# Kernel tuning notes

Measured on AMD Instinct MI355X. Metric: run time of the kernel, lower is better.

The kernel has to match this reference:

```python
import jax, jax.numpy as jnp
import numpy as np

NUM_HEADS = 8
MAX_REL = 32  # max_relative_positions
LN_EPS = 1e-5


def _conv1x1(x, W, b):
    # x: (B, C, H, W), W: (Cout, Cin), b: (Cout,)
    return jnp.einsum('bchw,oc->bohw', x, W) + b[None, :, None, None]


def setup_inputs() -> dict:
    key = jax.random.key(0)
    ks = jax.random.split(key, 10)
    B, C, H, W = 2, 512, 48, 48
    L = H * W
    s = 1.0 / np.sqrt(C)
    inp = {
        'x': jax.random.normal(ks[0], (B, C, H, W), jnp.float32),
        'mask': jax.random.randint(ks[1], (1, NUM_HEADS, L, L), 0, 2).astype(bool),
        'learnable_pos': jax.random.normal(ks[2], (1, C, H, W), jnp.float32) * 0.02,
        'Wq': jax.random.normal(ks[3], (C, C), jnp.float32) * s,
        'bq': jnp.zeros((C,), jnp.float32),
        'Wk': jax.random.normal(ks[4], (C, C), jnp.float32) * s,
        'bk': jnp.zeros((C,), jnp.float32),
        'Wv': jax.random.normal(ks[5], (C, C), jnp.float32) * s,
        'bv': jnp.zeros((C,), jnp.float32),
        'Wo': jax.random.normal(ks[6], (C, C), jnp.float32) * s,
        'bo': jnp.zeros((C,), jnp.float32),
        'rel_table': jax.random.normal(ks[7], (NUM_HEADS, 2 * MAX_REL + 1), jnp.float32) * 0.02,
        'ln_gamma': jnp.ones((C,), jnp.float32),
        'ln_beta': jnp.zeros((C,), jnp.float32),
    }
    return inp


def reference(x, mask, learnable_pos, Wq, bq, Wk, bk, Wv, bv, Wo, bo,
              rel_table, ln_gamma, ln_beta):
    B, C, H, W = x.shape
    L = H * W
    hd = C // NUM_HEADS
    residual = x

    xp = x + learnable_pos
    q = _conv1x1(xp, Wq, bq)
    k = _conv1x1(xp, Wk, bk)
    v = _conv1x1(xp, Wv, bv)

    def split_heads(t):  # (B,C,H,W) -> (B, heads, L, hd)
        return t.reshape(B, NUM_HEADS, hd, L).transpose(0, 1, 3, 2)

    q, k, v = split_heads(q), split_heads(k), split_heads(v)

    scale = 1.0 / np.sqrt(hd).astype(np.float32)
    scores = jnp.einsum('bhld,bhmd->bhlm', q, k) * scale  # (B,H,L,L)

    # relative positional bias per head
    pos = jnp.arange(L)
    rp = jnp.clip(pos[:, None] - pos[None, :], -MAX_REL, MAX_REL) + MAX_REL  # (L,L)
    scores = scores + rel_table[:, rp][None]  # (1,heads,L,L) broadcast

    scores = jnp.where(mask, scores, jnp.float32(-1e9))
    attn = jax.nn.softmax(scores, axis=-1)

    out = jnp.einsum('bhlm,bhmd->bhld', attn, v)  # (B,heads,L,hd)
    out = out.transpose(0, 1, 3, 2).reshape(B, C, H, W)
    out = _conv1x1(out, Wo, bo)

    y = residual + out
    # LayerNorm over channels (channels-last permute in original)
    yl = y.transpose(0, 2, 3, 1)  # (B,H,W,C)
    mu = jnp.mean(yl, axis=-1, keepdims=True)
    var = jnp.var(yl, axis=-1, keepdims=True)
    yl = (yl - mu) * jax.lax.rsqrt(var + LN_EPS) * ln_gamma + ln_beta
    return yl.transpose(0, 3, 1, 2)
```

## Files before the change

kernel.cpp:

```cpp
#include <hip/hip_runtime.h>
#include <cstdint>

#define L_SEQ 2304
#define CDIM  512
#define NHEADS 8
#define HD    64
#define LL    ((size_t)L_SEQ * L_SEQ)
#define ROWS_TOT (16 * L_SEQ)
#define PERBL ((size_t)2 * L_SEQ * 512)

typedef short  s8v  __attribute__((ext_vector_type(8)));
typedef float  f4v  __attribute__((ext_vector_type(4)));

__device__ __forceinline__ ushort f2bf(float f) {
    union { float f; uint32_t u; } v; v.f = f;
    uint32_t u = v.u;
    uint32_t r = (u + 0x7FFFu + ((u >> 16) & 1u)) >> 16;
    return (ushort)r;
}

__device__ __forceinline__ float bf2f(ushort u) {
    union { uint32_t u; float f; } v; v.u = (uint32_t)u << 16;
    return v.f;
}

__global__ __launch_bounds__(256) void prep_w(
    const float* __restrict__ Wq, const float* __restrict__ Wk,
    const float* __restrict__ Wv, const float* __restrict__ Wo,
    ushort* __restrict__ wb)
{
    const int i   = blockIdx.x * 256 + threadIdx.x;
    const int mat = i >> 16;
    const int j   = i & 65535;
    const float* src = (mat == 0) ? Wq : (mat == 1) ? Wk : (mat == 2) ? Wv : Wo;
    const float4 w = ((const float4*)src)[j];
    ushort4 o;
    o.x = f2bf(w.x); o.y = f2bf(w.y); o.z = f2bf(w.z); o.w = f2bf(w.w);
    ((ushort4*)(wb + (size_t)mat * 262144))[j] = o;
}

__global__ __launch_bounds__(256) void xpose(
    const float* __restrict__ x, const float* __restrict__ pos,
    ushort* __restrict__ xt)
{
    __shared__ ushort T[64][72];
    const int l0 = blockIdx.x * 64;
    const int c0 = blockIdx.y * 64;
    const int b  = blockIdx.z;
    const int t  = threadIdx.x;
    const int cc = t >> 2;
    const int l4 = (t & 3) * 16;
    const size_t off  = ((size_t)b * CDIM + c0 + cc) * L_SEQ + l0 + l4;
    const size_t poff = (size_t)(c0 + cc) * L_SEQ + l0 + l4;
    #pragma unroll
    for (int j4 = 0; j4 < 4; j4++) {
        const float4 xv = *(const float4*)&x[off + j4 * 4];
        const float4 pv = *(const float4*)&pos[poff + j4 * 4];
        T[cc][l4 + j4 * 4 + 0] = f2bf(xv.x + pv.x);
        T[cc][l4 + j4 * 4 + 1] = f2bf(xv.y + pv.y);
        T[cc][l4 + j4 * 4 + 2] = f2bf(xv.z + pv.z);
        T[cc][l4 + j4 * 4 + 3] = f2bf(xv.w + pv.w);
    }
    __syncthreads();
    const int lr = t >> 2;
    const int c4 = (t & 3) * 16;
    ushort o[16];
    #pragma unroll
    for (int j = 0; j < 16; j++) o[j] = T[c4 + j][lr];
    ushort* dst = &xt[((size_t)b * L_SEQ + l0 + lr) * 512 + c0 + c4];
    *(ushort4*)&dst[0]  = *(ushort4*)&o[0];
    *(ushort4*)&dst[4]  = *(ushort4*)&o[4];
    *(ushort4*)&dst[8]  = *(ushort4*)&o[8];
    *(ushort4*)&dst[12] = *(ushort4*)&o[12];
}

__global__ __launch_bounds__(256) void qkv_mfma(
    const ushort* __restrict__ xt, const ushort* __restrict__ wb,
    const float* __restrict__ bq, const float* __restrict__ bk,
    const float* __restrict__ bv,
    ushort* __restrict__ q_t, ushort* __restrict__ k_t, ushort* __restrict__ v_t)
{
    __shared__ __align__(16) ushort Bs[1024 * 8];
    const int l0  = blockIdx.x * 64;
    const int o0  = blockIdx.y * 64;
    const int b   = blockIdx.z / 3;
    const int mat = blockIdx.z % 3;
    const int t = threadIdx.x, w = t >> 6, lane = t & 63;
    const int n16 = lane & 15, q4 = lane >> 4;

    const ushort* A = xt + ((size_t)b * L_SEQ + l0 + w * 16 + n16) * 512 + q4 * 8;
    const ushort* W = wb + (size_t)mat * 262144;

    int sRow[4], sCol[4];
    #pragma unroll
    for (int i = 0; i < 4; i++) {
        const int c  = t + 256 * i;
        const int fr = c >> 6, ln = c & 63;
        sRow[i] = o0 + (fr & 3) * 16 + (ln & 15);
        sCol[i] = (fr >> 2) * 32 + (ln >> 4) * 8;
    }

    f4v acc[4] = {{0.f,0.f,0.f,0.f},{0.f,0.f,0.f,0.f},{0.f,0.f,0.f,0.f},{0.f,0.f,0.f,0.f}};
    for (int kb = 0; kb < 512; kb += 128) {
        __syncthreads();
        #pragma unroll
        for (int i = 0; i < 4; i++) {
            const int c = t + 256 * i;
            *(s8v*)&Bs[c * 8] = *(const s8v*)&W[(size_t)sRow[i] * 512 + kb + sCol[i]];
        }
        __syncthreads();
        #pragma unroll
        for (int ks = 0; ks < 4; ks++) {
            const s8v a = *(const s8v*)&A[kb + ks * 32];
            #pragma unroll
            for (int t4 = 0; t4 < 4; t4++) {
                const s8v bf = *(const s8v*)&Bs[((ks * 4 + t4) * 64 + lane) * 8];
                acc[t4] = __builtin_amdgcn_mfma_f32_16x16x32_bf16(a, bf, acc[t4], 0, 0, 0);
            }
        }
    }

    const float* bias = (mat == 0) ? bq : (mat == 1) ? bk : bv;
    const int h = o0 >> 6;
    const int rowbase = l0 + w * 16 + q4 * 4;

    if (mat < 2) {
        const float sc = (mat == 0) ? 0.125f : 1.0f;
        ushort* op = (mat == 0 ? q_t : k_t) + ((size_t)(b * NHEADS + h)) * L_SEQ * HD;
        #pragma unroll
        for (int t4 = 0; t4 < 4; t4++) {
            const float bi = bias[o0 + t4 * 16 + n16];
            #pragma unroll
            for (int r = 0; r < 4; r++)
                op[(size_t)(rowbase + r) * HD + t4 * 16 + n16] = f2bf((acc[t4][r] + bi) * sc);
        }
    } else {
        ushort* op = v_t + ((size_t)(b * NHEADS + h)) * HD * L_SEQ;
        #pragma unroll
        for (int t4 = 0; t4 < 4; t4++) {
            const float bi = bias[o0 + t4 * 16 + n16];
            ushort4 st;
            st.x = f2bf(acc[t4][0] + bi);
            st.y = f2bf(acc[t4][1] + bi);
            st.z = f2bf(acc[t4][2] + bi);
            st.w = f2bf(acc[t4][3] + bi);
            *(ushort4*)&op[(size_t)(t4 * 16 + n16) * L_SEQ + rowbase] = st;
        }
    }
}

__global__ __launch_bounds__(256) void flash_attn_mfma(
    const ushort* __restrict__ q, const ushort* __restrict__ k,
    const ushort* __restrict__ vt, const int* __restrict__ mask,
    const float* __restrict__ rel_table, ushort* __restrict__ Opart,
    float* __restrict__ Mpart, float* __restrict__ Lpart)
{
    __shared__ __align__(16) ushort Kf[512 * 8];
    __shared__ __align__(16) ushort Vf[512 * 8];
    __shared__ __align__(16) ushort Pb[4 * 16 * 72];
    __shared__ float rt[65];

    const int t    = threadIdx.x;
    const int id   = blockIdx.x;
    const int h    = id & 7;
    const int s2   = id >> 3;
    const int b    = s2 & 1;
    const int half = (s2 >> 1) & 1;
    const int qb   = s2 >> 2;
    const int bh   = b * NHEADS + h;
    const int l0   = qb * 64;
    const int w    = t >> 6;
    const int lane = t & 63;
    const int n16  = lane & 15;
    const int q4   = lane >> 4;

    if (t < 65) rt[t] = rel_table[h * 65 + t];

    const ushort* qp = q  + (size_t)bh * L_SEQ * HD;
    const ushort* kp = k  + (size_t)bh * L_SEQ * HD;
    const ushort* vp = vt + (size_t)bh * HD * L_SEQ;
    const int*    mp = mask + (size_t)h * LL;

    const int qrow = l0 + w * 16 + n16;
    const s8v qA0 = *(const s8v*)&qp[(size_t)qrow * HD + q4 * 8];
    const s8v qA1 = *(const s8v*)&qp[(size_t)qrow * HD + 32 + q4 * 8];

    f4v O[4] = {{0.f,0.f,0.f,0.f},{0.f,0.f,0.f,0.f},{0.f,0.f,0.f,0.f},{0.f,0.f,0.f,0.f}};
    float mrun[4] = {-3e38f, -3e38f, -3e38f, -3e38f};
    float lrun[4] = {0.f, 0.f, 0.f, 0.f};

    int sT[2], sS[2], sQ[2], sN[2];
    #pragma unroll
    for (int cc = 0; cc < 2; cc++) {
        const int c = t + cc * 256;
        const int g = c >> 6;
        sT[cc] = g >> 1; sS[cc] = g & 1;
        sQ[cc] = (c >> 4) & 3; sN[cc] = c & 15;
    }

    const int rowbase = l0 + w * 16 + q4 * 4;
    const int kbase = half * 1152;

    for (int mt = 0; mt < 18; mt++) {
        const int mb = kbase + mt * 64;
        __syncthreads();
        #pragma unroll
        for (int cc = 0; cc < 2; cc++) {
            const int c = t + cc * 256;
            const int key = sT[cc] * 16 + sN[cc];
            const int d0  = sS[cc] * 32 + sQ[cc] * 8;
            *(s8v*)&Kf[c * 8] = *(const s8v*)&kp[(size_t)(mb + key) * HD + d0];
            const int dd = sT[cc] * 16 + sN[cc];
            *(s8v*)&Vf[c * 8] = *(const s8v*)&vp[(size_t)dd * L_SEQ + mb + d0];
        }
        __syncthreads();

        int mreg[4][4];
        #pragma unroll
        for (int t4 = 0; t4 < 4; t4++)
            #pragma unroll
            for (int r = 0; r < 4; r++)
                mreg[t4][r] = mp[(size_t)(rowbase + r) * L_SEQ + mb + t4 * 16 + n16];

        f4v S[4];
        #pragma unroll
        for (int t4 = 0; t4 < 4; t4++) {
            const s8v b0 = *(const s8v*)&Kf[((t4 * 2 + 0) * 64 + lane) * 8];
            const s8v b1 = *(const s8v*)&Kf[((t4 * 2 + 1) * 64 + lane) * 8];
            f4v acc = {0.f, 0.f, 0.f, 0.f};
            acc = __builtin_amdgcn_mfma_f32_16x16x32_bf16(qA0, b0, acc, 0, 0, 0);
            acc = __builtin_amdgcn_mfma_f32_16x16x32_bf16(qA1, b1, acc, 0, 0, 0);
            S[t4] = acc;
        }

        #pragma unroll
        for (int t4 = 0; t4 < 4; t4++) {
            const int A = (l0 + w * 16) - (mb + t4 * 16);
            if (A >= 47) {
                const float bu = rt[64];
                #pragma unroll
                for (int r = 0; r < 4; r++) S[t4][r] += bu;
            } else if (A <= -47) {
                const float bu = rt[0];
                #pragma unroll
                for (int r = 0; r < 4; r++) S[t4][r] += bu;
            } else {
                #pragma unroll
                for (int r = 0; r < 4; r++) {
                    int dix = A + q4 * 4 + r - n16;
                    dix = min(max(dix, -32), 32) + 32;
                    S[t4][r] += rt[dix];
                }
            }
            #pragma unroll
            for (int r = 0; r < 4; r++)
                if (mreg[t4][r] == 0) S[t4][r] = -1e9f;
        }

        float mx[4];
        #pragma unroll
        for (int r = 0; r < 4; r++) {
            float m0 = fmaxf(fmaxf(S[0][r], S[1][r]), fmaxf(S[2][r], S[3][r]));
            m0 = fmaxf(m0, __shfl_xor(m0, 1));
            m0 = fmaxf(m0, __shfl_xor(m0, 2));
            m0 = fmaxf(m0, __shfl_xor(m0, 4));
            m0 = fmaxf(m0, __shfl_xor(m0, 8));
            mx[r] = m0;
        }
        float al[4];
        #pragma unroll
        for (int r = 0; r < 4; r++) {
            const float mn = fmaxf(mrun[r], mx[r]);
            al[r] = __expf(mrun[r] - mn);
            mrun[r] = mn;
            float sum = 0.f;
            #pragma unroll
            for (int t4 = 0; t4 < 4; t4++) {
                const float p = __expf(S[t4][r] - mn);
                S[t4][r] = p;
                sum += p;
                Pb[w * 1152 + (q4 * 4 + r) * 72 + t4 * 16 + n16] = f2bf(p);
            }
            sum += __shfl_xor(sum, 1);
            sum += __shfl_xor(sum, 2);
            sum += __shfl_xor(sum, 4);
            sum += __shfl_xor(sum, 8);
            lrun[r] = lrun[r] * al[r] + sum;
        }

        const s8v pf0 = *(const s8v*)&Pb[w * 1152 + n16 * 72 + q4 * 8];
        const s8v pf1 = *(const s8v*)&Pb[w * 1152 + n16 * 72 + 32 + q4 * 8];
        #pragma unroll
        for (int t4 = 0; t4 < 4; t4++) {
            f4v o = O[t4];
            #pragma unroll
            for (int r = 0; r < 4; r++) o[r] *= al[r];
            const s8v v0 = *(const s8v*)&Vf[((t4 * 2 + 0) * 64 + lane) * 8];
            const s8v v1 = *(const s8v*)&Vf[((t4 * 2 + 1) * 64 + lane) * 8];
            o = __builtin_amdgcn_mfma_f32_16x16x32_bf16(pf0, v0, o, 0, 0, 0);
            o = __builtin_amdgcn_mfma_f32_16x16x32_bf16(pf1, v1, o, 0, 0, 0);
            O[t4] = o;
        }
    }

    ushort* op = Opart + (size_t)half * PERBL + (size_t)b * L_SEQ * 512;
    #pragma unroll
    for (int r = 0; r < 4; r++) {
        const size_t base = (size_t)(rowbase + r) * 512 + h * 64;
        #pragma unroll
        for (int t4 = 0; t4 < 4; t4++)
            op[base + t4 * 16 + n16] = f2bf(O[t4][r]);
    }
    if (n16 == 0) {
        const size_t sb = (size_t)half * ROWS_TOT + (size_t)bh * L_SEQ;
        #pragma unroll
        for (int r = 0; r < 4; r++) {
            Mpart[sb + rowbase + r] = mrun[r];
            Lpart[sb + rowbase + r] = lrun[r];
        }
    }
}

__global__ __launch_bounds__(256) void combine_kernel(
    const ushort* __restrict__ O01, const float* __restrict__ Mp,
    const float* __restrict__ Lp, ushort* __restrict__ at)
{
    const int i   = blockIdx.x * 256 + threadIdx.x;
    const int c8  = i & 63;
    const int row = i >> 6;
    const int b   = row / L_SEQ;
    const int l   = row - b * L_SEQ;
    const int h   = c8 >> 3;
    const size_t s = (size_t)(b * NHEADS + h) * L_SEQ + l;
    const float m0 = Mp[s], m1 = Mp[ROWS_TOT + s];
    const float l0 = Lp[s], l1 = Lp[ROWS_TOT + s];
    const float M  = fmaxf(m0, m1);
    const float w0 = __expf(m0 - M);
    const float w1 = __expf(m1 - M);
    const float inv = 1.0f / (l0 * w0 + l1 * w1);
    const float f0 = w0 * inv;
    const float f1 = w1 * inv;
    const size_t o = (size_t)row * 512 + c8 * 8;
    const ushort4 a0 = *(const ushort4*)&O01[o];
    const ushort4 a1 = *(const ushort4*)&O01[o + 4];
    const ushort4 c0 = *(const ushort4*)&O01[PERBL + o];
    const ushort4 c1 = *(const ushort4*)&O01[PERBL + o + 4];
    ushort4 r0, r1;
    r0.x = f2bf(bf2f(a0.x) * f0 + bf2f(c0.x) * f1);
    r0.y = f2bf(bf2f(a0.y) * f0 + bf2f(c0.y) * f1);
    r0.z = f2bf(bf2f(a0.z) * f0 + bf2f(c0.z) * f1);
    r0.w = f2bf(bf2f(a0.w) * f0 + bf2f(c0.w) * f1);
    r1.x = f2bf(bf2f(a1.x) * f0 + bf2f(c1.x) * f1);
    r1.y = f2bf(bf2f(a1.y) * f0 + bf2f(c1.y) * f1);
    r1.z = f2bf(bf2f(a1.z) * f0 + bf2f(c1.z) * f1);
    r1.w = f2bf(bf2f(a1.w) * f0 + bf2f(c1.w) * f1);
    *(ushort4*)&at[o]     = r0;
    *(ushort4*)&at[o + 4] = r1;
}

__global__ __launch_bounds__(256) void out_mfma(
    const ushort* __restrict__ at, const ushort* __restrict__ wb,
    const float* __restrict__ bo, const float* __restrict__ x,
    float* __restrict__ y)
{
    __shared__ __align__(16) ushort Bs[1024 * 8];
    const int l0 = blockIdx.x * 64;
    const int o0 = blockIdx.y * 64;
    const int b  = blockIdx.z;
    const int t = threadIdx.x, w = t >> 6, lane = t & 63;
    const int n16 = lane & 15, q4 = lane >> 4;

    const ushort* A = at + ((size_t)b * L_SEQ + l0 + w * 16 + n16) * 512 + q4 * 8;
    const ushort* W = wb + (size_t)3 * 262144;

    int sRow[4], sCol[4];
    #pragma unroll
    for (int i = 0; i < 4; i++) {
        const int c  = t + 256 * i;
        const int fr = c >> 6, ln = c & 63;
        sRow[i] = o0 + (fr & 3) * 16 + (ln & 15);
        sCol[i] = (fr >> 2) * 32 + (ln >> 4) * 8;
    }

    f4v acc[4] = {{0.f,0.f,0.f,0.f},{0.f,0.f,0.f,0.f},{0.f,0.f,0.f,0.f},{0.f,0.f,0.f,0.f}};
    for (int kb = 0; kb < 512; kb += 128) {
        __syncthreads();
        #pragma unroll
        for (int i = 0; i < 4; i++) {
            const int c = t + 256 * i;
            *(s8v*)&Bs[c * 8] = *(const s8v*)&W[(size_t)sRow[i] * 512 + kb + sCol[i]];
        }
        __syncthreads();
        #pragma unroll
        for (int ks = 0; ks < 4; ks++) {
            const s8v a = *(const s8v*)&A[kb + ks * 32];
            #pragma unroll
            for (int t4 = 0; t4 < 4; t4++) {
                const s8v bf = *(const s8v*)&Bs[((ks * 4 + t4) * 64 + lane) * 8];
                acc[t4] = __builtin_amdgcn_mfma_f32_16x16x32_bf16(a, bf, acc[t4], 0, 0, 0);
            }
        }
    }

    const int rowbase = l0 + w * 16 + q4 * 4;
    #pragma unroll
    for (int t4 = 0; t4 < 4; t4++) {
        const int o = o0 + t4 * 16 + n16;
        const float bi = bo[o];
        const size_t off = ((size_t)b * CDIM + o) * L_SEQ + rowbase;
        const float4 xv = *(const float4*)&x[off];
        float4 st;
        st.x = acc[t4][0] + bi + xv.x;
        st.y = acc[t4][1] + bi + xv.y;
        st.z = acc[t4][2] + bi + xv.z;
        st.w = acc[t4][3] + bi + xv.w;
        *(float4*)&y[off] = st;
    }
}

__global__ __launch_bounds__(256) void ln_kernel(
    float* __restrict__ y, const float* __restrict__ gamma,
    const float* __restrict__ beta)
{
    const int t = threadIdx.x;
    const int p = t & 15;
    const int g = t >> 4;
    const int pos = blockIdx.x * 16 + p;
    const int b = (pos >= L_SEQ) ? 1 : 0;
    const int l = pos - b * L_SEQ;
    float* col = y + (size_t)b * CDIM * L_SEQ + l;

    float s = 0.f, sq = 0.f;
    for (int c = g * 32; c < g * 32 + 32; c++) {
        const float v = col[(size_t)c * L_SEQ];
        s += v; sq += v * v;
    }
    __shared__ float S1[16][16];
    __shared__ float S2[16][16];
    S1[g][p] = s; S2[g][p] = sq;
    __syncthreads();
    if (t < 16) {
        float ss = 0.f, qq = 0.f;
        #pragma unroll
        for (int gg = 0; gg < 16; gg++) { ss += S1[gg][t]; qq += S2[gg][t]; }
        const float mu = ss * (1.0f / CDIM);
        const float var = qq * (1.0f / CDIM) - mu * mu;
        S1[0][t] = mu;
        S2[0][t] = rsqrtf(var + 1e-5f);
    }
    __syncthreads();
    const float mu = S1[0][p];
    const float rs = S2[0][p];
    for (int c = g * 32; c < g * 32 + 32; c++) {
        const float v = col[(size_t)c * L_SEQ];
        col[(size_t)c * L_SEQ] = (v - mu) * rs * gamma[c] + beta[c];
    }
}

extern "C" void kernel_launch(void* const* d_in, const int* in_sizes, int n_in,
                              void* d_out, int out_size, void* d_ws, size_t ws_size,
                              hipStream_t stream) {
    const float* x    = (const float*)d_in[0];
    const int* mask   = (const int*)d_in[1];
    const float* pos  = (const float*)d_in[2];
    const float* Wq   = (const float*)d_in[3];
    const float* bq   = (const float*)d_in[4];
    const float* Wk   = (const float*)d_in[5];
    const float* bk   = (const float*)d_in[6];
    const float* Wv   = (const float*)d_in[7];
    const float* bv   = (const float*)d_in[8];
    const float* Wo   = (const float*)d_in[9];
    const float* bo   = (const float*)d_in[10];
    const float* rel  = (const float*)d_in[11];
    const float* gam  = (const float*)d_in[12];
    const float* bet  = (const float*)d_in[13];

    ushort* qw  = (ushort*)d_ws;
    ushort* kw  = qw + PERBL;
    ushort* vw  = kw + PERBL;
    ushort* xtw = vw + PERBL;
    ushort* wbw = xtw + PERBL;
    ushort* Opart = wbw + (size_t)4 * 512 * 512;
    float* Mpart = (float*)(Opart + 2 * PERBL);
    float* Lpart = Mpart + 2 * ROWS_TOT;
    ushort* attnT = xtw;
    float* y = (float*)d_out;

    prep_w<<<dim3(1024), 256, 0, stream>>>(Wq, Wk, Wv, Wo, wbw);

    xpose<<<dim3(L_SEQ / 64, CDIM / 64, 2), 256, 0, stream>>>(x, pos, xtw);

    qkv_mfma<<<dim3(L_SEQ / 64, CDIM / 64, 6), 256, 0, stream>>>(
        xtw, wbw, bq, bk, bv, qw, kw, vw);

    flash_attn_mfma<<<dim3(1152), 256, 0, stream>>>(qw, kw, vw, mask, rel,
                                                    Opart, Mpart, Lpart);

    combine_kernel<<<dim3(1152), 256, 0, stream>>>(Opart, Mpart, Lpart, attnT);

    out_mfma<<<dim3(L_SEQ / 64, CDIM / 64, 2), 256, 0, stream>>>(
        attnT, wbw, bo, x, y);

    ln_kernel<<<(2 * L_SEQ) / 16, 256, 0, stream>>>(y, gam, bet);
}
```

Measured before the change: 396.2 us.

## Fuse Q/K/V projections per block, register-prefetch weights, widen LN tile

The QKV projection kernel now computes all three output matrices in one block, so the activation tile is loaded once into registers (16 fragments) and reused across Q, K and V. Weight tiles are prefetched into registers for the next k-step while MFMAs run on the current shared-memory tile. The output projection gets the same A-register and B-prefetch treatment. The LayerNorm kernel processes 32 positions per block instead of 16, for wider coalesced accesses. The trade-off is higher register and LDS use (three B tiles) and a third as many QKV blocks, which may lower occupancy.

```diff
diff --git a/kernel.cpp b/kernel.cpp
--- a/kernel.cpp
+++ b/kernel.cpp
@@ -80,70 +80,89 @@
     const float* __restrict__ bv,
     ushort* __restrict__ q_t, ushort* __restrict__ k_t, ushort* __restrict__ v_t)
 {
-    __shared__ __align__(16) ushort Bs[1024 * 8];
+    __shared__ __align__(16) ushort Bs[3][1024 * 8];
     const int l0  = blockIdx.x * 64;
     const int o0  = blockIdx.y * 64;
-    const int b   = blockIdx.z / 3;
-    const int mat = blockIdx.z % 3;
+    const int b   = blockIdx.z;
     const int t = threadIdx.x, w = t >> 6, lane = t & 63;
     const int n16 = lane & 15, q4 = lane >> 4;
 
     const ushort* A = xt + ((size_t)b * L_SEQ + l0 + w * 16 + n16) * 512 + q4 * 8;
-    const ushort* W = wb + (size_t)mat * 262144;
-
-    int sRow[4], sCol[4];
+
+    s8v areg[16];
+    #pragma unroll
+    for (int i = 0; i < 16; i++) areg[i] = *(const s8v*)&A[i * 32];
+
+    int sOff[4];
     #pragma unroll
     for (int i = 0; i < 4; i++) {
         const int c  = t + 256 * i;
         const int fr = c >> 6, ln = c & 63;
-        sRow[i] = o0 + (fr & 3) * 16 + (ln & 15);
-        sCol[i] = (fr >> 2) * 32 + (ln >> 4) * 8;
-    }
-
-    f4v acc[4] = {{0.f,0.f,0.f,0.f},{0.f,0.f,0.f,0.f},{0.f,0.f,0.f,0.f},{0.f,0.f,0.f,0.f}};
+        sOff[i] = (o0 + (fr & 3) * 16 + (ln & 15)) * 512 + (fr >> 2) * 32 + (ln >> 4) * 8;
+    }
+
+    s8v breg[3][4];
+    #pragma unroll
+    for (int m = 0; m < 3; m++)
+        #pragma unroll
+        for (int i = 0; i < 4; i++)
+            breg[m][i] = *(const s8v*)&wb[(size_t)m * 262144 + sOff[i]];
+
+    f4v acc[3][4] = {};
     for (int kb = 0; kb < 512; kb += 128) {
         __syncthreads();
         #pragma unroll
-        for (int i = 0; i < 4; i++) {
-            const int c = t + 256 * i;
-            *(s8v*)&Bs[c * 8] = *(const s8v*)&W[(size_t)sRow[i] * 512 + kb + sCol[i]];
-        }
+        for (int m = 0; m < 3; m++)
+            #pragma unroll
+            for (int i = 0; i < 4; i++)
+                *(s8v*)&Bs[m][(t + 256 * i) * 8] = breg[m][i];
         __syncthreads();
+        if (kb < 384) {
+            #pragma unroll
+            for (int m = 0; m < 3; m++)
+                #pragma unroll
+                for (int i = 0; i < 4; i++)
+                    breg[m][i] = *(const s8v*)&wb[(size_t)m * 262144 + sOff[i] + kb + 128];
+        }
         #pragma unroll
         for (int ks = 0; ks < 4; ks++) {
-            const s8v a = *(const s8v*)&A[kb + ks * 32];
-            #pragma unroll
-            for (int t4 = 0; t4 < 4; t4++) {
-                const s8v bf = *(const s8v*)&Bs[((ks * 4 + t4) * 64 + lane) * 8];
-                acc[t4] = __builtin_amdgcn_mfma_f32_16x16x32_bf16(a, bf, acc[t4], 0, 0, 0);
-            }
-        }
-    }
-
-    const float* bias = (mat == 0) ? bq : (mat == 1) ? bk : bv;
+            const s8v a = areg[(kb >> 5) + ks];
+            #pragma unroll
+            for (int m = 0; m < 3; m++)
+                #pragma unroll
+                for (int t4 = 0; t4 < 4; t4++) {
+                    const s8v bf = *(const s8v*)&Bs[m][((ks * 4 + t4) * 64 + lane) * 8];
+                    acc[m][t4] = __builtin_amdgcn_mfma_f32_16x16x32_bf16(a, bf, acc[m][t4], 0, 0, 0);
+                }
+        }
+    }
+
     const int h = o0 >> 6;
     const int rowbase = l0 + w * 16 + q4 * 4;
 
-    if (mat < 2) {
-        const float sc = (mat == 0) ? 0.125f : 1.0f;
-        ushort* op = (mat == 0 ? q_t : k_t) + ((size_t)(b * NHEADS + h)) * L_SEQ * HD;
+    #pragma unroll
+    for (int m = 0; m < 2; m++) {
+        const float* bias = (m == 0) ? bq : bk;
+        const float sc = (m == 0) ? 0.125f : 1.0f;
+        ushort* op = (m == 0 ? q_t : k_t) + ((size_t)(b * NHEADS + h)) * L_SEQ * HD;
         #pragma unroll
         for (int t4 = 0; t4 < 4; t4++) {
             const float bi = bias[o0 + t4 * 16 + n16];
             #pragma unroll
             for (int r = 0; r < 4; r++)
-                op[(size_t)(rowbase + r) * HD + t4 * 16 + n16] = f2bf((acc[t4][r] + bi) * sc);
-        }
-    } else {
+                op[(size_t)(rowbase + r) * HD + t4 * 16 + n16] = f2bf((acc[m][t4][r] + bi) * sc);
+        }
+    }
+    {
         ushort* op = v_t + ((size_t)(b * NHEADS + h)) * HD * L_SEQ;
         #pragma unroll
         for (int t4 = 0; t4 < 4; t4++) {
-            const float bi = bias[o0 + t4 * 16 + n16];
+            const float bi = bv[o0 + t4 * 16 + n16];
             ushort4 st;
-            st.x = f2bf(acc[t4][0] + bi);
-            st.y = f2bf(acc[t4][1] + bi);
-            st.z = f2bf(acc[t4][2] + bi);
-            st.w = f2bf(acc[t4][3] + bi);
+            st.x = f2bf(acc[2][t4][0] + bi);
+            st.y = f2bf(acc[2][t4][1] + bi);
+            st.z = f2bf(acc[2][t4][2] + bi);
+            st.w = f2bf(acc[2][t4][3] + bi);
             *(ushort4*)&op[(size_t)(t4 * 16 + n16) * L_SEQ + rowbase] = st;
         }
     }
@@ -373,27 +392,37 @@
     const ushort* A = at + ((size_t)b * L_SEQ + l0 + w * 16 + n16) * 512 + q4 * 8;
     const ushort* W = wb + (size_t)3 * 262144;
 
-    int sRow[4], sCol[4];
+    s8v areg[16];
+    #pragma unroll
+    for (int i = 0; i < 16; i++) areg[i] = *(const s8v*)&A[i * 32];
+
+    int sOff[4];
     #pragma unroll
     for (int i = 0; i < 4; i++) {
         const int c  = t + 256 * i;
         const int fr = c >> 6, ln = c & 63;
-        sRow[i] = o0 + (fr & 3) * 16 + (ln & 15);
-        sCol[i] = (fr >> 2) * 32 + (ln >> 4) * 8;
-    }
+        sOff[i] = (o0 + (fr & 3) * 16 + (ln & 15)) * 512 + (fr >> 2) * 32 + (ln >> 4) * 8;
+    }
+
+    s8v breg[4];
+    #pragma unroll
+    for (int i = 0; i < 4; i++) breg[i] = *(const s8v*)&W[sOff[i]];
 
     f4v acc[4] = {{0.f,0.f,0.f,0.f},{0.f,0.f,0.f,0.f},{0.f,0.f,0.f,0.f},{0.f,0.f,0.f,0.f}};
     for (int kb = 0; kb < 512; kb += 128) {
         __syncthreads();
         #pragma unroll
-        for (int i = 0; i < 4; i++) {
-            const int c = t + 256 * i;
-            *(s8v*)&Bs[c * 8] = *(const s8v*)&W[(size_t)sRow[i] * 512 + kb + sCol[i]];
-        }
+        for (int i = 0; i < 4; i++)
+            *(s8v*)&Bs[(t + 256 * i) * 8] = breg[i];
         __syncthreads();
+        if (kb < 384) {
+            #pragma unroll
+            for (int i = 0; i < 4; i++)
+                breg[i] = *(const s8v*)&W[sOff[i] + kb + 128];
+        }
         #pragma unroll
         for (int ks = 0; ks < 4; ks++) {
-            const s8v a = *(const s8v*)&A[kb + ks * 32];
+            const s8v a = areg[(kb >> 5) + ks];
             #pragma unroll
             for (int t4 = 0; t4 < 4; t4++) {
                 const s8v bf = *(const s8v*)&Bs[((ks * 4 + t4) * 64 + lane) * 8];
@@ -423,26 +452,26 @@
     const float* __restrict__ beta)
 {
     const int t = threadIdx.x;
-    const int p = t & 15;
-    const int g = t >> 4;
-    const int pos = blockIdx.x * 16 + p;
+    const int p = t & 31;
+    const int g = t >> 5;
+    const int pos = blockIdx.x * 32 + p;
     const int b = (pos >= L_SEQ) ? 1 : 0;
     const int l = pos - b * L_SEQ;
     float* col = y + (size_t)b * CDIM * L_SEQ + l;
 
     float s = 0.f, sq = 0.f;
-    for (int c = g * 32; c < g * 32 + 32; c++) {
+    for (int c = g * 64; c < g * 64 + 64; c++) {
         const float v = col[(size_t)c * L_SEQ];
         s += v; sq += v * v;
     }
-    __shared__ float S1[16][16];
-    __shared__ float S2[16][16];
+    __shared__ float S1[8][32];
+    __shared__ float S2[8][32];
     S1[g][p] = s; S2[g][p] = sq;
     __syncthreads();
-    if (t < 16) {
+    if (t < 32) {
         float ss = 0.f, qq = 0.f;
         #pragma unroll
-        for (int gg = 0; gg < 16; gg++) { ss += S1[gg][t]; qq += S2[gg][t]; }
+        for (int gg = 0; gg < 8; gg++) { ss += S1[gg][t]; qq += S2[gg][t]; }
         const float mu = ss * (1.0f / CDIM);
         const float var = qq * (1.0f / CDIM) - mu * mu;
         S1[0][t] = mu;
@@ -451,7 +480,7 @@
     __syncthreads();
     const float mu = S1[0][p];
     const float rs = S2[0][p];
-    for (int c = g * 32; c < g * 32 + 32; c++) {
+    for (int c = g * 64; c < g * 64 + 64; c++) {
         const float v = col[(size_t)c * L_SEQ];
         col[(size_t)c * L_SEQ] = (v - mu) * rs * gamma[c] + beta[c];
     }
@@ -490,7 +519,7 @@
 
     xpose<<<dim3(L_SEQ / 64, CDIM / 64, 2), 256, 0, stream>>>(x, pos, xtw);
 
-    qkv_mfma<<<dim3(L_SEQ / 64, CDIM / 64, 6), 256, 0, stream>>>(
+    qkv_mfma<<<dim3(L_SEQ / 64, CDIM / 64, 2), 256, 0, stream>>>(
         xtw, wbw, bq, bk, bv, qw, kw, vw);
 
     flash_attn_mfma<<<dim3(1152), 256, 0, stream>>>(qw, kw, vw, mask, rel,
@@ -501,5 +530,5 @@
     out_mfma<<<dim3(L_SEQ / 64, CDIM / 64, 2), 256, 0, stream>>>(
         attnT, wbw, bo, x, y);
 
-    ln_kernel<<<(2 * L_SEQ) / 16, 256, 0, stream>>>(y, gam, bet);
-}
+    ln_kernel<<<(2 * L_SEQ) / 32, 256, 0, stream>>>(y, gam, bet);
+}
```

Measured after the change: 394.9 us. About the same (-0.3%).
